# Kernel tuning notes

Hardware: AMD Instinct MI355X
Metric: run time of the kernel (lower is better)

Reference implementation:

```python
import jax, jax.numpy as jnp
import numpy as np

B, S, D = 2, 2048, 2048
H, HKV = 32, 8
HD = D // H  # 64
NEG_INF = -1e9


def _rope_tables(seq_len, head_dim):
    inv_freq = 1.0 / (10000.0 ** (np.arange(0, head_dim, 2, dtype=np.float32) / head_dim))
    t = np.arange(seq_len, dtype=np.float32)
    freqs = np.outer(t, inv_freq)                      # (S, HD/2)
    emb = np.concatenate([freqs, freqs], axis=-1)      # (S, HD)
    cos = np.cos(emb)[None, None]                      # (1,1,S,HD)
    sin = np.sin(emb)[None, None]
    return jnp.asarray(cos), jnp.asarray(sin)


def setup_inputs() -> dict:
    key = jax.random.key(0)
    ks = jax.random.split(key, 5)
    hidden_states = jax.random.normal(ks[0], (B, S, D), dtype=jnp.float32)
    # causal additive mask: 0 where allowed, -inf (large negative) where masked
    causal = jnp.tril(jnp.ones((S, S), dtype=jnp.bool_))
    attention_mask = jnp.where(causal, 0.0, NEG_INF).astype(jnp.float32)
    attention_mask = jnp.broadcast_to(attention_mask[None, None], (B, 1, S, S))
    cos, sin = _rope_tables(S, HD)
    sc = 0.02
    Wq = jax.random.normal(ks[1], (D, H * HD), dtype=jnp.float32) * sc
    Wk = jax.random.normal(ks[2], (D, HKV * HD), dtype=jnp.float32) * sc
    Wv = jax.random.normal(ks[3], (D, HKV * HD), dtype=jnp.float32) * sc
    Wo = jax.random.normal(ks[4], (H * HD, D), dtype=jnp.float32) * sc
    return {"hidden_states": hidden_states, "attention_mask": attention_mask,
            "cos": cos, "sin": sin, "Wq": Wq, "Wk": Wk, "Wv": Wv, "Wo": Wo}


def _rotate_half(x):
    x1, x2 = jnp.split(x, 2, axis=-1)
    return jnp.concatenate([-x2, x1], axis=-1)


def _apply_rope(x, cos, sin):
    # x: (B, h, S, HD); cos/sin: (1,1,S,HD)
    return x * cos + _rotate_half(x) * sin


def reference(hidden_states, attention_mask, cos, sin, Wq, Wk, Wv, Wo):
    b, s, _ = hidden_states.shape
    scale = 1.0 / np.sqrt(HD)
    q = (hidden_states @ Wq).reshape(b, s, H, HD).transpose(0, 2, 1, 3)    # (B,H,S,HD)
    k = (hidden_states @ Wk).reshape(b, s, HKV, HD).transpose(0, 2, 1, 3)  # (B,HKV,S,HD)
    v = (hidden_states @ Wv).reshape(b, s, HKV, HD).transpose(0, 2, 1, 3)
    q = _apply_rope(q, cos, sin)
    k = _apply_rope(k, cos, sin)
    # GQA: group query heads per kv head without materializing repeated KV
    g = H // HKV
    qg = q.reshape(b, HKV, g, s, HD)
    scores = jnp.einsum('bkgqd,bksd->bkgqs', qg, k) * scale               # (B,HKV,g,S,S)
    scores = scores + attention_mask[:, :, None]                          # broadcast (B,1,1,S,S)
    attn = jax.nn.softmax(scores, axis=-1)
    out = jnp.einsum('bkgqs,bksd->bkgqd', attn, v)                        # (B,HKV,g,S,HD)
    out = out.reshape(b, H, s, HD).transpose(0, 2, 1, 3).reshape(b, s, H * HD)
    return out @ Wo
```

## Files before the change

kernel.cpp:

```cpp
#include <hip/hip_runtime.h>
#include <math.h>

typedef _Float16 half8 __attribute__((ext_vector_type(8)));
typedef _Float16 half4 __attribute__((ext_vector_type(4)));
typedef _Float16 half2 __attribute__((ext_vector_type(2)));
typedef float f32x4 __attribute__((ext_vector_type(4)));

#define S_LEN 2048
#define DM    2048
#define NH    32
#define NKV   8

#define QSCALE 0.1803368801111204f
#define NSHIFT -11.541560327111707f

#if __has_builtin(__builtin_amdgcn_exp2f)
#define EXP2(x) __builtin_amdgcn_exp2f(x)
#else
#define EXP2(x) __builtin_exp2f(x)
#endif

__device__ __forceinline__ half2 pkrtz(float a, float b) {
    return __builtin_bit_cast(half2, __builtin_amdgcn_cvt_pkrtz(a, b));
}

__device__ __forceinline__ void async16(const void* g, void* l) {
    __builtin_amdgcn_global_load_lds(
        (const __attribute__((address_space(1))) unsigned int*)g,
        (__attribute__((address_space(3))) unsigned int*)l, 16, 0, 0);
}

__global__ __launch_bounds__(256) void cast_h(const float* __restrict__ x,
                                              _Float16* __restrict__ y, int n)
{
    int i = (blockIdx.x * 256 + threadIdx.x) * 4;
    if (i >= n) return;
    float4 v = *(const float4*)(x + i);
    half4 o = {(_Float16)v.x, (_Float16)v.y, (_Float16)v.z, (_Float16)v.w};
    *(half4*)(y + i) = o;
}

__global__ __launch_bounds__(256) void transpose_all(
    const float* __restrict__ Wq, const float* __restrict__ Wk,
    const float* __restrict__ Wv, const float* __restrict__ Wo,
    _Float16* __restrict__ Wqkv_t, _Float16* __restrict__ Wo_t)
{
    const int z = blockIdx.z;
    const float* W; _Float16* Wt; int N;
    if (z == 0)      { W = Wq; Wt = Wqkv_t;                        N = 2048; }
    else if (z == 1) { W = Wk; Wt = Wqkv_t + (size_t)2048 * 2048;  N = 512;  }
    else if (z == 2) { W = Wv; Wt = Wqkv_t + (size_t)2560 * 2048;  N = 512;  }
    else             { W = Wo; Wt = Wo_t;                          N = 2048; }
    if ((int)blockIdx.x * 32 >= N) return;

    __shared__ float t[32][33];
    const int n0 = blockIdx.x * 32, k0 = blockIdx.y * 32;
    const int tx = threadIdx.x & 31, ty = threadIdx.x >> 5;
#pragma unroll
    for (int i = 0; i < 32; i += 8)
        t[ty + i][tx] = W[(size_t)(k0 + ty + i) * N + n0 + tx];
    __syncthreads();
#pragma unroll
    for (int i = 0; i < 32; i += 8)
        Wt[(size_t)(n0 + ty + i) * 2048 + k0 + tx] = (_Float16)t[tx][ty + i];
}

#define LSW64(basep, row, halfofs) \
    (*(const half8*)((basep) + (row) * 64 + (((((halfofs) >> 3) & 7) ^ ((row) & 7)) << 3)))

__global__ __launch_bounds__(256) void gemm_h(
    const _Float16* __restrict__ A, const _Float16* __restrict__ Bt,
    void* __restrict__ Cout, int N, int K, int mode,
    const float* __restrict__ cosT, const float* __restrict__ sinT)
{
    __shared__ __align__(16) _Float16 Al[128 * 64];
    __shared__ __align__(16) _Float16 Bl[128 * 64];
    const int tid = threadIdx.x;
    const int bm = blockIdx.y * 128, bn = blockIdx.x * 128;
    const int wave = tid >> 6, lane = tid & 63;
    const int wm = (wave & 1) * 64, wn = (wave >> 1) * 64;
    const int lm = lane & 15, quad = lane >> 4;

    int ro[4], co[4];
#pragma unroll
    for (int u = 0; u < 4; ++u) {
        const int f = u * 4096 + tid * 16;
        ro[u] = f >> 7;
        co[u] = ((f >> 4) & 7) ^ (ro[u] & 7);
    }

    f32x4 acc[4][4];
#pragma unroll
    for (int i = 0; i < 4; ++i)
#pragma unroll
        for (int j = 0; j < 4; ++j) acc[i][j] = (f32x4){0.f, 0.f, 0.f, 0.f};

    for (int k0 = 0; k0 < K; k0 += 64) {
#pragma unroll
        for (int u = 0; u < 4; ++u) {
            async16(A + (size_t)(bm + ro[u]) * K + k0 + co[u] * 8,
                    (char*)Al + u * 4096 + tid * 16);
            async16(Bt + (size_t)(bn + ro[u]) * K + k0 + co[u] * 8,
                    (char*)Bl + u * 4096 + tid * 16);
        }
        __syncthreads();
#pragma unroll
        for (int kp = 0; kp < 2; ++kp) {
            half8 af[4], bf[4];
#pragma unroll
            for (int i = 0; i < 4; ++i)
                af[i] = LSW64(Al, wm + i * 16 + lm, kp * 32 + quad * 8);
#pragma unroll
            for (int j = 0; j < 4; ++j)
                bf[j] = LSW64(Bl, wn + j * 16 + lm, kp * 32 + quad * 8);
#pragma unroll
            for (int i = 0; i < 4; ++i)
#pragma unroll
                for (int j = 0; j < 4; ++j)
                    acc[i][j] = __builtin_amdgcn_mfma_f32_16x16x32_f16(af[i], bf[j], acc[i][j], 0, 0, 0);
        }
        __syncthreads();
    }

    const int mrow = bm + wm + quad * 4;
    if (mode == 0) {
        float* C = (float*)Cout;
        const int col0 = bn + wn + lm;
#pragma unroll
        for (int i = 0; i < 4; ++i)
#pragma unroll
            for (int r = 0; r < 4; ++r) {
                int m = mrow + i * 16 + r;
#pragma unroll
                for (int j = 0; j < 4; ++j)
                    C[(size_t)m * N + col0 + j * 16] = acc[i][j][r];
            }
        return;
    }

    _Float16* Cq = (_Float16*)Cout;
    _Float16* Ck = Cq + (size_t)2 * NH * S_LEN * 64;
    _Float16* Cv = Ck + (size_t)2 * NKV * S_LEN * 64;
    const int colbase = bn + wn;
    const int region = (colbase >= 2560) ? 2 : (colbase >= 2048) ? 1 : 0;

    if (region == 2) {
        const int head = (colbase - 2560) >> 6;
#pragma unroll
        for (int i = 0; i < 4; ++i) {
            const int m0 = mrow + i * 16;
            const int b = m0 >> 11, s0 = m0 & 2047;
#pragma unroll
            for (int j = 0; j < 4; ++j) {
                half2 lo = pkrtz(acc[i][j][0], acc[i][j][1]);
                half2 hi = pkrtz(acc[i][j][2], acc[i][j][3]);
                half4 ov = {lo[0], lo[1], hi[0], hi[1]};
                *(half4*)(Cv + ((((size_t)b * NKV + head) << 6) + lm + j * 16) * S_LEN + s0) = ov;
            }
        }
        return;
    }

    const float qscale = (region == 0) ? QSCALE : 1.0f;
    const int head = (region == 0) ? (colbase >> 6) : ((colbase - 2048) >> 6);
    _Float16* Cdst = (region == 0) ? Cq : Ck;
    const int nh = (region == 0) ? NH : NKV;
#pragma unroll
    for (int i = 0; i < 4; ++i)
#pragma unroll
        for (int r = 0; r < 4; ++r) {
            int m = mrow + i * 16 + r;
            int b = m >> 11, s = m & 2047;
            const float* cp = cosT + s * 64 + lm;
            const float* sp = sinT + s * 64 + lm;
            float a0 = acc[i][0][r], a1 = acc[i][1][r], a2 = acc[i][2][r], a3 = acc[i][3][r];
            float o0 = (a0 * cp[0]  - a2 * sp[0])  * qscale;
            float o1 = (a1 * cp[16] - a3 * sp[16]) * qscale;
            float o2 = (a2 * cp[32] + a0 * sp[32]) * qscale;
            float o3 = (a3 * cp[48] + a1 * sp[48]) * qscale;
            _Float16* d = Cdst + ((((size_t)b * nh + head) * S_LEN + s) << 6) + lm;
            d[0]  = (_Float16)o0;
            d[16] = (_Float16)o1;
            d[32] = (_Float16)o2;
            d[48] = (_Float16)o3;
        }
}

#define LSWOFS(row, halfofs) \
    ((row) * 64 + (((((halfofs) >> 3) & 7) ^ ((row) & 7)) << 3) + ((halfofs) & 7))

__global__ __launch_bounds__(256, 2) void attn_h(
    const _Float16* __restrict__ q, const _Float16* __restrict__ k,
    const _Float16* __restrict__ vt, _Float16* __restrict__ x2)
{
    __shared__ __align__(16) _Float16 Ks[64 * 64];
    __shared__ __align__(16) _Float16 Vts[64 * 64];

    const int kvh = blockIdx.y, b = blockIdx.z;
    const int tid = threadIdx.x;
    const int wave = tid >> 6, lane = tid & 63;
    const int lm = lane & 15, quad = lane >> 4;
    const int h = kvh * 4 + wave;

    const int qtT[2] = {63 - (int)blockIdx.x, (int)blockIdx.x};
    const int ktm[2] = {(qtT[0] * 32 + 31) >> 6, (qtT[1] * 32 + 31) >> 6};

    const _Float16* kbase  = k  + ((((size_t)b * NKV + kvh) * S_LEN) << 6);
    const _Float16* vtbase = vt + ((((size_t)b * NKV + kvh) << 6) * S_LEN);

    half8 qf[2][2][2];
#pragma unroll
    for (int tp = 0; tp < 2; ++tp) {
        const _Float16* qb = q + ((((size_t)b * NH + h) * S_LEN + qtT[tp] * 32) << 6);
#pragma unroll
        for (int i = 0; i < 2; ++i)
#pragma unroll
            for (int kk = 0; kk < 2; ++kk)
                qf[tp][i][kk] = *(const half8*)(qb + (i * 16 + lm) * 64 + kk * 32 + quad * 8);
    }

    f32x4 accOT[2][2][4];
    float lpart[2][2];
#pragma unroll
    for (int tp = 0; tp < 2; ++tp)
#pragma unroll
        for (int i = 0; i < 2; ++i) {
            lpart[tp][i] = 0.f;
#pragma unroll
            for (int j = 0; j < 4; ++j) accOT[tp][i][j] = (f32x4){0.f, 0.f, 0.f, 0.f};
        }

    const int f0 = tid * 16, f1 = 4096 + tid * 16;
    const int r0 = f0 >> 7, r1 = f1 >> 7;
    const int c0 = ((f0 >> 4) & 7) ^ (r0 & 7);
    const int c1 = ((f1 >> 4) & 7) ^ (r1 & 7);

    for (int kt = 0; kt <= ktm[0]; ++kt) {
        async16((const char*)kbase + (size_t)kt * 8192 + r0 * 128 + c0 * 16, (char*)Ks + f0);
        async16((const char*)kbase + (size_t)kt * 8192 + r1 * 128 + c1 * 16, (char*)Ks + f1);
        async16((const char*)vtbase + (size_t)r0 * 4096 + kt * 128 + c0 * 16, (char*)Vts + f0);
        async16((const char*)vtbase + (size_t)r1 * 4096 + kt * 128 + c1 * 16, (char*)Vts + f1);
        __syncthreads();

        half8 kf[4][2];
        half4 vtf[4][4];
#pragma unroll
        for (int t = 0; t < 4; ++t) {
#pragma unroll
            for (int kk = 0; kk < 2; ++kk)
                kf[t][kk] = *(const half8*)(Ks + LSWOFS(t * 16 + lm, kk * 32 + quad * 8));
#pragma unroll
            for (int j = 0; j < 4; ++j)
                vtf[j][t] = *(const half4*)(Vts + LSWOFS(j * 16 + lm, t * 16 + quad * 4));
        }

#pragma unroll
        for (int tp = 0; tp < 2; ++tp) {
            if (kt > ktm[tp]) continue;
            const bool diag = (kt == ktm[tp]);
#pragma unroll
            for (int i = 0; i < 2; ++i) {
                f32x4 sc[4];
#pragma unroll
                for (int t = 0; t < 4; ++t) {
                    f32x4 z = (f32x4){NSHIFT, NSHIFT, NSHIFT, NSHIFT};
                    z = __builtin_amdgcn_mfma_f32_16x16x32_f16(kf[t][0], qf[tp][i][0], z, 0, 0, 0);
                    z = __builtin_amdgcn_mfma_f32_16x16x32_f16(kf[t][1], qf[tp][i][1], z, 0, 0, 0);
                    sc[t] = z;
                }
                if (diag) {
                    const int qpos = qtT[tp] * 32 + i * 16 + lm;
#pragma unroll
                    for (int t = 0; t < 4; ++t)
#pragma unroll
                        for (int r = 0; r < 4; ++r) {
                            int key = kt * 64 + t * 16 + quad * 4 + r;
                            if (key > qpos) sc[t][r] = -30000.f;
                        }
                }
                half4 pt[4];
                float lp = 0.f;
#pragma unroll
                for (int t = 0; t < 4; ++t) {
                    float p0 = EXP2(sc[t][0]), p1 = EXP2(sc[t][1]);
                    float p2 = EXP2(sc[t][2]), p3 = EXP2(sc[t][3]);
                    lp += (p0 + p1) + (p2 + p3);
                    half2 lo = pkrtz(p0, p1);
                    half2 hi = pkrtz(p2, p3);
                    pt[t] = (half4){lo[0], lo[1], hi[0], hi[1]};
                }
                lpart[tp][i] += lp;
#pragma unroll
                for (int j = 0; j < 4; ++j)
#pragma unroll
                    for (int t = 0; t < 4; ++t)
                        accOT[tp][i][j] = __builtin_amdgcn_mfma_f32_16x16x16f16(
                            vtf[j][t], pt[t], accOT[tp][i][j], 0, 0, 0);
            }
        }
        __syncthreads();
    }

#pragma unroll
    for (int tp = 0; tp < 2; ++tp)
#pragma unroll
        for (int i = 0; i < 2; ++i) {
            float l = lpart[tp][i];
            l += __shfl_xor(l, 16);
            l += __shfl_xor(l, 32);
            const float inv = 1.f / l;
            const size_t row = (size_t)b * S_LEN + qtT[tp] * 32 + i * 16 + lm;
#pragma unroll
            for (int j = 0; j < 4; ++j) {
                f32x4 o = accOT[tp][i][j];
                half2 lo = pkrtz(o[0] * inv, o[1] * inv);
                half2 hi = pkrtz(o[2] * inv, o[3] * inv);
                half4 ov = {lo[0], lo[1], hi[0], hi[1]};
                *(half4*)(x2 + row * DM + h * 64 + j * 16 + quad * 4) = ov;
            }
        }
}

extern "C" void kernel_launch(void* const* d_in, const int* in_sizes, int n_in,
                              void* d_out, int out_size, void* d_ws, size_t ws_size,
                              hipStream_t stream)
{
    const float* hidden = (const float*)d_in[0];
    const float* cosT = (const float*)d_in[2];
    const float* sinT = (const float*)d_in[3];
    const float* Wq = (const float*)d_in[4];
    const float* Wk = (const float*)d_in[5];
    const float* Wv = (const float*)d_in[6];
    const float* Wo = (const float*)d_in[7];
    float* out = (float*)d_out;

    _Float16* w = (_Float16*)d_ws;
    _Float16* hid_h  = w;  w += (size_t)4096 * 2048;
    _Float16* Wqkv_t = w;  w += (size_t)3072 * 2048;
    _Float16* Wo_t   = w;  w += (size_t)2048 * 2048;
    _Float16* qh     = w;  w += (size_t)2 * NH * S_LEN * 64;
    _Float16* kh     = w;  w += (size_t)2 * NKV * S_LEN * 64;
    _Float16* vth    = w;  w += (size_t)2 * NKV * S_LEN * 64;
    _Float16* x2h    = w;

    dim3 blk(256);
    cast_h<<<dim3(8192), blk, 0, stream>>>(hidden, hid_h, 8388608);
    transpose_all<<<dim3(64, 64, 4), blk, 0, stream>>>(Wq, Wk, Wv, Wo, Wqkv_t, Wo_t);

    gemm_h<<<dim3(24, 32), blk, 0, stream>>>(hid_h, Wqkv_t, qh, 3072, 2048, 1, cosT, sinT);

    attn_h<<<dim3(32, 8, 2), blk, 0, stream>>>(qh, kh, vth, x2h);

    gemm_h<<<dim3(16, 32), blk, 0, stream>>>(x2h, Wo_t, out, 2048, 2048, 0, nullptr, nullptr);
}
```

Baseline: 350.2 us.

## Rewrite GEMM as 256x256-tile, 8-wave, double-buffered pipelined kernel

The fp16 GEMM moves from 128x128 tiles with 4 waves and single-buffered LDS to 256x256 tiles with 8 waves, each wave computing 128x64. K tiles are staged in double-buffered LDS in 32-wide halves, with async loads interleaved between MFMA phases and guarded by explicit vmcnt waits, barriers and s_setprio. The aim is to hide global-load latency and raise MFMA density per LDS read. In exchange, grids shrink to 192 and 128 blocks on a 256-CU part, which leaves many CUs idle, and register pressure rises.

```diff
diff --git a/kernel.cpp b/kernel.cpp
--- a/kernel.cpp
+++ b/kernel.cpp
@@ -65,75 +65,111 @@
         Wt[(size_t)(n0 + ty + i) * 2048 + k0 + tx] = (_Float16)t[tx][ty + i];
 }
 
-#define LSW64(basep, row, halfofs) \
-    (*(const half8*)((basep) + (row) * 64 + (((((halfofs) >> 3) & 7) ^ ((row) & 7)) << 3)))
-
-__global__ __launch_bounds__(256) void gemm_h(
+__global__ __launch_bounds__(512, 2) void gemm_h(
     const _Float16* __restrict__ A, const _Float16* __restrict__ Bt,
     void* __restrict__ Cout, int N, int K, int mode,
     const float* __restrict__ cosT, const float* __restrict__ sinT)
 {
-    __shared__ __align__(16) _Float16 Al[128 * 64];
-    __shared__ __align__(16) _Float16 Bl[128 * 64];
-    const int tid = threadIdx.x;
-    const int bm = blockIdx.y * 128, bn = blockIdx.x * 128;
-    const int wave = tid >> 6, lane = tid & 63;
-    const int wm = (wave & 1) * 64, wn = (wave >> 1) * 64;
+    __shared__ __align__(16) _Float16 Lds[2][4][8192];
+    const int tid  = threadIdx.x;
+    const int lane = tid & 63;
+    const int wave = tid >> 6;
     const int lm = lane & 15, quad = lane >> 4;
-
-    int ro[4], co[4];
-#pragma unroll
-    for (int u = 0; u < 4; ++u) {
-        const int f = u * 4096 + tid * 16;
-        ro[u] = f >> 7;
-        co[u] = ((f >> 4) & 7) ^ (ro[u] & 7);
-    }
-
-    f32x4 acc[4][4];
-#pragma unroll
-    for (int i = 0; i < 4; ++i)
+    const int wm = wave >> 2;
+    const int wn = wave & 3;
+    const int bm = blockIdx.y * 256, bn = blockIdx.x * 256;
+    const int nt = K >> 6;
+
+    const int rr = tid >> 2;
+    const int c8 = (((tid & 3) ^ (rr & 3)) << 3);
+    const _Float16* pA0 = A  + (size_t)(bm + rr)       * K + c8;
+    const _Float16* pA1 = A  + (size_t)(bm + 128 + rr) * K + c8;
+    const _Float16* pB0 = Bt + (size_t)(bn + rr)       * K + c8;
+    const _Float16* pB1 = Bt + (size_t)(bn + 128 + rr) * K + c8;
+    char* ldsb = (char*)Lds + tid * 16;
+
+#define STAGE(t, idx) do { if ((t) < nt) {                          \
+        const int koff_ = (t) * 64 + (((idx) >> 1) << 5);           \
+        char* d_ = ldsb + (((t) & 1) << 16) + ((idx) << 14);        \
+        async16((((idx) & 1) ? pA0 : pB0) + koff_, d_);             \
+        async16((((idx) & 1) ? pA1 : pB1) + koff_, d_ + 8192);      \
+    } } while (0)
+
+    const int chq = ((quad ^ (lm & 3)) << 3);
+    const _Float16* Lh = (const _Float16*)Lds;
+    const int a0 = (wm << 7) + lm;
+    const int b0 = (wn << 6) + lm;
+
+    f32x4 acc[8][4];
+#pragma unroll
+    for (int i = 0; i < 8; ++i)
 #pragma unroll
         for (int j = 0; j < 4; ++j) acc[i][j] = (f32x4){0.f, 0.f, 0.f, 0.f};
 
-    for (int k0 = 0; k0 < K; k0 += 64) {
-#pragma unroll
-        for (int u = 0; u < 4; ++u) {
-            async16(A + (size_t)(bm + ro[u]) * K + k0 + co[u] * 8,
-                    (char*)Al + u * 4096 + tid * 16);
-            async16(Bt + (size_t)(bn + ro[u]) * K + k0 + co[u] * 8,
-                    (char*)Bl + u * 4096 + tid * 16);
-        }
-        __syncthreads();
-#pragma unroll
-        for (int kp = 0; kp < 2; ++kp) {
-            half8 af[4], bf[4];
-#pragma unroll
-            for (int i = 0; i < 4; ++i)
-                af[i] = LSW64(Al, wm + i * 16 + lm, kp * 32 + quad * 8);
-#pragma unroll
-            for (int j = 0; j < 4; ++j)
-                bf[j] = LSW64(Bl, wn + j * 16 + lm, kp * 32 + quad * 8);
-#pragma unroll
-            for (int i = 0; i < 4; ++i)
-#pragma unroll
-                for (int j = 0; j < 4; ++j)
-                    acc[i][j] = __builtin_amdgcn_mfma_f32_16x16x32_f16(af[i], bf[j], acc[i][j], 0, 0, 0);
-        }
-        __syncthreads();
-    }
-
-    const int mrow = bm + wm + quad * 4;
+    STAGE(0, 0); STAGE(0, 1); STAGE(0, 2); STAGE(0, 3);
+    STAGE(1, 0); STAGE(1, 1); STAGE(1, 2);
+    if (nt > 1) asm volatile("s_waitcnt vmcnt(6)" ::: "memory");
+    else        asm volatile("s_waitcnt vmcnt(0)" ::: "memory");
+    __builtin_amdgcn_s_barrier();
+
+    half8 af[4], bf[4];
+#define MFMA16(mb)                                                            \
+    _Pragma("unroll") for (int i_ = 0; i_ < 4; ++i_)                          \
+    _Pragma("unroll") for (int j_ = 0; j_ < 4; ++j_)                          \
+        acc[(mb) + i_][j_] = __builtin_amdgcn_mfma_f32_16x16x32_f16(          \
+            af[i_], bf[j_], acc[(mb) + i_][j_], 0, 0, 0);
+
+#define PH_BAR()  __builtin_amdgcn_s_barrier();                               \
+                  asm volatile("s_waitcnt lgkmcnt(0)" ::: "memory");          \
+                  __builtin_amdgcn_s_setprio(1)
+#define PH_END()  __builtin_amdgcn_s_setprio(0);                              \
+                  __builtin_amdgcn_s_barrier()
+
+    int p = 0;
+    for (int G = 0; G < nt; ++G, p ^= 1) {
+        const _Float16* Lp = Lh + (p << 15);
+#pragma unroll
+        for (int i = 0; i < 4; ++i) af[i] = *(const half8*)(Lp + 8192  + (a0 + i * 16) * 32 + chq);
+#pragma unroll
+        for (int j = 0; j < 4; ++j) bf[j] = *(const half8*)(Lp +         (b0 + j * 16) * 32 + chq);
+        STAGE(G + 1, 3);
+        PH_BAR(); MFMA16(0); PH_END();
+#pragma unroll
+        for (int i = 0; i < 4; ++i) af[i] = *(const half8*)(Lp + 8192  + (a0 + 64 + i * 16) * 32 + chq);
+        STAGE(G + 2, 0);
+        PH_BAR(); MFMA16(4); PH_END();
+#pragma unroll
+        for (int i = 0; i < 4; ++i) af[i] = *(const half8*)(Lp + 24576 + (a0 + i * 16) * 32 + chq);
+#pragma unroll
+        for (int j = 0; j < 4; ++j) bf[j] = *(const half8*)(Lp + 16384 + (b0 + j * 16) * 32 + chq);
+        STAGE(G + 2, 1);
+        PH_BAR(); MFMA16(0); PH_END();
+#pragma unroll
+        for (int i = 0; i < 4; ++i) af[i] = *(const half8*)(Lp + 24576 + (a0 + 64 + i * 16) * 32 + chq);
+        STAGE(G + 2, 2);
+        PH_BAR(); MFMA16(4);
+        __builtin_amdgcn_s_setprio(0);
+        if (G + 2 < nt) asm volatile("s_waitcnt vmcnt(6)" ::: "memory");
+        else            asm volatile("s_waitcnt vmcnt(0)" ::: "memory");
+        __builtin_amdgcn_s_barrier();
+    }
+#undef STAGE
+#undef MFMA16
+#undef PH_BAR
+#undef PH_END
+
+    const int mrowq = bm + (wm << 7) + (quad << 2);
     if (mode == 0) {
         float* C = (float*)Cout;
-        const int col0 = bn + wn + lm;
-#pragma unroll
-        for (int i = 0; i < 4; ++i)
+        const int col0 = bn + (wn << 6) + lm;
+#pragma unroll
+        for (int mf = 0; mf < 8; ++mf)
 #pragma unroll
             for (int r = 0; r < 4; ++r) {
-                int m = mrow + i * 16 + r;
-#pragma unroll
-                for (int j = 0; j < 4; ++j)
-                    C[(size_t)m * N + col0 + j * 16] = acc[i][j][r];
+                const int m = mrowq + mf * 16 + r;
+#pragma unroll
+                for (int nf = 0; nf < 4; ++nf)
+                    C[(size_t)m * N + col0 + nf * 16] = acc[mf][nf][r];
             }
         return;
     }
@@ -141,21 +177,21 @@
     _Float16* Cq = (_Float16*)Cout;
     _Float16* Ck = Cq + (size_t)2 * NH * S_LEN * 64;
     _Float16* Cv = Ck + (size_t)2 * NKV * S_LEN * 64;
-    const int colbase = bn + wn;
+    const int colbase = bn + (wn << 6);
     const int region = (colbase >= 2560) ? 2 : (colbase >= 2048) ? 1 : 0;
 
     if (region == 2) {
         const int head = (colbase - 2560) >> 6;
 #pragma unroll
-        for (int i = 0; i < 4; ++i) {
-            const int m0 = mrow + i * 16;
+        for (int mf = 0; mf < 8; ++mf) {
+            const int m0 = mrowq + mf * 16;
             const int b = m0 >> 11, s0 = m0 & 2047;
 #pragma unroll
-            for (int j = 0; j < 4; ++j) {
-                half2 lo = pkrtz(acc[i][j][0], acc[i][j][1]);
-                half2 hi = pkrtz(acc[i][j][2], acc[i][j][3]);
+            for (int nf = 0; nf < 4; ++nf) {
+                half2 lo = pkrtz(acc[mf][nf][0], acc[mf][nf][1]);
+                half2 hi = pkrtz(acc[mf][nf][2], acc[mf][nf][3]);
                 half4 ov = {lo[0], lo[1], hi[0], hi[1]};
-                *(half4*)(Cv + ((((size_t)b * NKV + head) << 6) + lm + j * 16) * S_LEN + s0) = ov;
+                *(half4*)(Cv + ((((size_t)b * NKV + head) << 6) + lm + nf * 16) * S_LEN + s0) = ov;
             }
         }
         return;
@@ -166,18 +202,19 @@
     _Float16* Cdst = (region == 0) ? Cq : Ck;
     const int nh = (region == 0) ? NH : NKV;
 #pragma unroll
-    for (int i = 0; i < 4; ++i)
+    for (int mf = 0; mf < 8; ++mf)
 #pragma unroll
         for (int r = 0; r < 4; ++r) {
-            int m = mrow + i * 16 + r;
+            int m = mrowq + mf * 16 + r;
             int b = m >> 11, s = m & 2047;
             const float* cp = cosT + s * 64 + lm;
             const float* sp = sinT + s * 64 + lm;
-            float a0 = acc[i][0][r], a1 = acc[i][1][r], a2 = acc[i][2][r], a3 = acc[i][3][r];
-            float o0 = (a0 * cp[0]  - a2 * sp[0])  * qscale;
-            float o1 = (a1 * cp[16] - a3 * sp[16]) * qscale;
-            float o2 = (a2 * cp[32] + a0 * sp[32]) * qscale;
-            float o3 = (a3 * cp[48] + a1 * sp[48]) * qscale;
+            float a0r = acc[mf][0][r], a1r = acc[mf][1][r];
+            float a2r = acc[mf][2][r], a3r = acc[mf][3][r];
+            float o0 = (a0r * cp[0]  - a2r * sp[0])  * qscale;
+            float o1 = (a1r * cp[16] - a3r * sp[16]) * qscale;
+            float o2 = (a2r * cp[32] + a0r * sp[32]) * qscale;
+            float o3 = (a3r * cp[48] + a1r * sp[48]) * qscale;
             _Float16* d = Cdst + ((((size_t)b * nh + head) * S_LEN + s) << 6) + lm;
             d[0]  = (_Float16)o0;
             d[16] = (_Float16)o1;
@@ -347,9 +384,9 @@
     cast_h<<<dim3(8192), blk, 0, stream>>>(hidden, hid_h, 8388608);
     transpose_all<<<dim3(64, 64, 4), blk, 0, stream>>>(Wq, Wk, Wv, Wo, Wqkv_t, Wo_t);
 
-    gemm_h<<<dim3(24, 32), blk, 0, stream>>>(hid_h, Wqkv_t, qh, 3072, 2048, 1, cosT, sinT);
+    gemm_h<<<dim3(12, 16), dim3(512), 0, stream>>>(hid_h, Wqkv_t, qh, 3072, 2048, 1, cosT, sinT);
 
     attn_h<<<dim3(32, 8, 2), blk, 0, stream>>>(qh, kh, vth, x2h);
 
-    gemm_h<<<dim3(16, 32), blk, 0, stream>>>(x2h, Wo_t, out, 2048, 2048, 0, nullptr, nullptr);
-}
+    gemm_h<<<dim3(8, 16), dim3(512), 0, stream>>>(x2h, Wo_t, out, 2048, 2048, 0, nullptr, nullptr);
+}
```

After: 333.2 us. 1.05x faster.
